# Optimization experiments

Hardware: AMD Instinct MI355X
Metric: run time of the kernel (lower is better)

## Reference

```python
import jax, jax.numpy as jnp
import numpy as np
from jax import lax

D_MODEL = 1024
N_HEADS = 16
D_HEAD = D_MODEL // N_HEADS  # 64
NB_FEAT = 266
CHUNK = 128
KERNEL_EPS = 1e-4
CAUSAL_EPS = 1e-6


def _gaussian_orthogonal_matrix(nb_rows, nb_cols, seed=0):
    # Performer gaussian_orthogonal_random_matrix, scaling=0:
    # stacked orthogonal blocks scaled by chi-distributed row norms.
    rng = np.random.default_rng(seed)
    blocks = []
    n_full = nb_rows // nb_cols + (1 if nb_rows % nb_cols else 0)
    for _ in range(n_full):
        g = rng.standard_normal((nb_cols, nb_cols))
        q_mat, _ = np.linalg.qr(g)
        blocks.append(q_mat.T)
    mat = np.concatenate(blocks, axis=0)[:nb_rows]
    multiplier = np.linalg.norm(rng.standard_normal((nb_rows, nb_cols)), axis=1)
    return jnp.asarray((multiplier[:, None] * mat).astype(np.float32))


def setup_inputs() -> dict:
    key = jax.random.key(0)
    ks = jax.random.split(key, 9)
    s = 1.0 / np.sqrt(D_MODEL)
    x = jax.random.normal(ks[0], (2, 4096, D_MODEL), dtype=jnp.float32)
    def lin(k):
        kw, kb = jax.random.split(k)
        W = jax.random.uniform(kw, (D_MODEL, D_MODEL), jnp.float32, -s, s)
        b = jax.random.uniform(kb, (D_MODEL,), jnp.float32, -s, s)
        return W, b
    Wq, bq = lin(ks[1]); Wk, bk = lin(ks[2]); Wv, bv = lin(ks[3]); Wo, bo = lin(ks[4])
    proj = _gaussian_orthogonal_matrix(NB_FEAT, D_HEAD)
    return {"x": x, "Wq": Wq, "bq": bq, "Wk": Wk, "bk": bk, "Wv": Wv, "bv": bv,
            "Wo": Wo, "bo": bo, "proj": proj}


def _softmax_kernel(data, proj, is_query):
    # Performer random-feature softmax kernel.
    data_normalizer = data.shape[-1] ** -0.25
    ratio = proj.shape[0] ** -0.5
    dn = data * data_normalizer  # [b,h,n,d]
    data_dash = jnp.einsum('bhnd,md->bhnm', dn, proj)
    diag = 0.5 * jnp.sum(dn * dn, axis=-1, keepdims=True)  # [b,h,n,1]
    if is_query:
        stab = jnp.max(data_dash, axis=-1, keepdims=True)
    else:
        stab = jnp.max(data_dash)
    return ratio * (jnp.exp(data_dash - diag - stab) + KERNEL_EPS)


def _causal_linear_attention(qp, kp, v, chunk_size):
    # Chunked O(n) causal linear attention (Performer noncuda variant).
    b, h, n, m = qp.shape
    d = v.shape[-1]
    nc = n // chunk_size
    qc = jnp.moveaxis(qp.reshape(b, h, nc, chunk_size, m), 2, 0)  # [nc,b,h,c,m]
    kc = jnp.moveaxis(kp.reshape(b, h, nc, chunk_size, m), 2, 0)
    vc = jnp.moveaxis(v.reshape(b, h, nc, chunk_size, d), 2, 0)   # [nc,b,h,c,d]

    def step(carry, inp):
        last_k, last_ctx = carry  # [b,h,m], [b,h,m,d]
        q, k, vv = inp
        k_cum = last_k[:, :, None, :] + jnp.cumsum(k, axis=-2)          # [b,h,c,m]
        D_inv = 1.0 / jnp.einsum('bhcm,bhcm->bhc', q, k_cum + CAUSAL_EPS)
        ctx = jnp.einsum('bhcm,bhcd->bhcmd', k, vv)                     # [b,h,c,m,d]
        ctx_cum = last_ctx[:, :, None, :, :] + jnp.cumsum(ctx, axis=2)
        out = jnp.einsum('bhcmd,bhcm,bhc->bhcd', ctx_cum, q, D_inv)
        return (k_cum[:, :, -1, :], ctx_cum[:, :, -1, :, :]), out

    carry0 = (jnp.zeros((b, h, m), qp.dtype), jnp.zeros((b, h, m, d), qp.dtype))
    _, outs = lax.scan(step, carry0, (qc, kc, vc))  # [nc,b,h,c,d]
    return jnp.moveaxis(outs, 0, 2).reshape(b, h, n, d)


def reference(x, Wq, bq, Wk, bk, Wv, bv, Wo, bo, proj):
    bsz, n, _ = x.shape
    def split_heads(t):
        return t.reshape(bsz, n, N_HEADS, D_HEAD).transpose(0, 2, 1, 3)  # [b,h,n,d]
    q = split_heads(x @ Wq.T + bq)
    k = split_heads(x @ Wk.T + bk)
    v = split_heads(x @ Wv.T + bv)
    q_prime = _softmax_kernel(q, proj, is_query=True)
    k_prime = _softmax_kernel(k, proj, is_query=False)
    attn = _causal_linear_attention(q_prime, k_prime, v, CHUNK)  # [b,h,n,d]
    attn = attn.transpose(0, 2, 1, 3).reshape(bsz, n, D_MODEL)
    return attn @ Wo.T + bo
```

## Files before the change

kernel.cpp:

```cpp
#include <hip/hip_runtime.h>

#define B_    2
#define NSEQ  4096
#define DM    1024
#define H_    16
#define DH    64
#define MF    266
#define MP    288
#define NROWS (B_*NSEQ)
#define NHROWS (B_*H_*NSEQ)
#define RATIO 0.06131393394849658f
#define DNORM 0.3535533905932738f
#define KEPS  1e-4f
#define CEPS  1e-6f

#define CH    128
#define NC    32
#define SROW  (65*MP)
#define SELEM (64*MP)

#define AS1 __attribute__((address_space(1)))
#define AS3 __attribute__((address_space(3)))

typedef unsigned short u16;
typedef unsigned int   u32;

typedef __bf16 bf16x8 __attribute__((ext_vector_type(8)));
typedef float  f32x4  __attribute__((ext_vector_type(4)));

__device__ __forceinline__ float b2f(u16 u){ u32 x = ((u32)u) << 16; return __builtin_bit_cast(float, x); }
__device__ __forceinline__ u16 f2b(float f){
    u32 x = __builtin_bit_cast(u32, f);
    u32 r = x + 0x7fffu + ((x >> 16) & 1u);
    return (u16)(r >> 16);
}
__device__ __forceinline__ u32 enc_max(float f){ u32 b = __builtin_bit_cast(u32, f); return (b & 0x80000000u) ? ~b : (b | 0x80000000u); }
__device__ __forceinline__ float dec_max(u32 u){ u32 b = (u & 0x80000000u) ? (u & 0x7fffffffu) : ~u; return __builtin_bit_cast(float, b); }

struct DetectArgs { const u32* p[10]; int nw[10]; };

__global__ void detect_all(DetectArgs a, u32* __restrict__ flags)
{
    __shared__ int cnt[256];
    int k = blockIdx.x;
    const u32* src = a.p[k];
    int nwords = a.nw[k];
    int t = threadIdx.x; int c = 0;
    for (int i = t; i < nwords; i += 256) {
        u32 w = src[i];
        int ea = (int)((w >> 7)  & 0xFF);
        int eb = (int)((w >> 23) & 0xFF);
        c += (ea >= 112 && ea <= 143) ? 1 : 0;
        c += (eb >= 112 && eb <= 143) ? 1 : 0;
    }
    cnt[t] = c; __syncthreads();
    for (int s = 128; s; s >>= 1) { if (t < s) cnt[t] += cnt[t + s]; __syncthreads(); }
    if (t == 0) flags[k] = (cnt[0] >= (nwords * 3) / 2) ? 1u : 0u;
}

__device__ __forceinline__ void conv8(const void* src, u16* dst, int i, u32 flag)
{
    if (flag) {
        *(uint4*)(dst + i) = *(const uint4*)((const u16*)src + i);
    } else {
        const float* s = (const float*)src + i;
        u16 tmp[8];
        #pragma unroll
        for (int j = 0; j < 8; ++j) tmp[j] = f2b(s[j]);
        *(uint4*)(dst + i) = *(uint4*)tmp;
    }
}

struct ConvAllArgs {
    const void* xs;    u16* xd;
    const void* wsrc[4]; u16* wdst[4];
    const void* bsrc[4]; u16* bdst[4];
    const void* pj;    u16* pjd;
    u32* gpart; u32* gmax;
    const u32* flags;
};

__global__ __launch_bounds__(256)
void conv_all(ConvAllArgs a)
{
    int blk = blockIdx.x, t = threadIdx.x;
    if (blk < 4096) {
        int i = blk * 2048 + t * 8;
        conv8(a.xs, a.xd, i, a.flags[0]);
    } else if (blk < 6144) {
        int r = blk - 4096; int w = r >> 9; int i = (r & 511) * 2048 + t * 8;
        conv8(a.wsrc[w], a.wdst[w], i, a.flags[1 + 2*w]);
    } else if (blk < 6148) {
        int w = blk - 6144; int i = t * 8;
        if (i < DM) conv8(a.bsrc[w], a.bdst[w], i, a.flags[2 + 2*w]);
    } else if (blk < 6157) {
        int i = (blk - 6148) * 2048 + t * 8;
        if (i < MF * DH) conv8(a.pj, a.pjd, i, a.flags[9]);
        else             *(uint4*)(a.pjd + i) = (uint4){0,0,0,0};
    } else {
        a.gpart[t] = 0u;
        if (t == 0) *a.gmax = 0u;
    }
}

#define GEMM_BODY(A_, Bm_, ACC_)                                              \
    const int K = DM;                                                          \
    __shared__ u16 As[128 * 32];                                               \
    __shared__ u16 Bs[128 * 32];                                               \
    int t = threadIdx.x;                                                       \
    int wave = t >> 6, lane = t & 63;                                          \
    int wm = wave >> 1, wn = wave & 1;                                         \
    int quad = lane >> 4, l16 = lane & 15;                                     \
    int bm = blockIdx.x * 128, bn = blockIdx.y * 128;                          \
    int rA0 = (wave*2 + 0)*16 + (lane >> 2);                                   \
    int rA1 = (wave*2 + 1)*16 + (lane >> 2);                                   \
    int cs0 = ((lane & 3) ^ (rA0 & 3)) * 8;                                    \
    int cs1 = ((lane & 3) ^ (rA1 & 3)) * 8;                                    \
    const u16* a0 = A_  + (size_t)(bm + rA0) * K + cs0;                        \
    const u16* a1 = A_  + (size_t)(bm + rA1) * K + cs1;                        \
    const u16* b0 = Bm_ + (size_t)(bn + rA0) * K + cs0;                        \
    const u16* b1 = Bm_ + (size_t)(bn + rA1) * K + cs1;                        \
    u16* la0 = As + (wave*2 + 0)*512;                                          \
    u16* la1 = As + (wave*2 + 1)*512;                                          \
    u16* lb0 = Bs + (wave*2 + 0)*512;                                          \
    u16* lb1 = Bs + (wave*2 + 1)*512;                                          \
    f32x4 ACC_[4][4];                                                          \
    _Pragma("unroll")                                                          \
    for (int i = 0; i < 4; ++i)                                                \
        _Pragma("unroll")                                                      \
        for (int j = 0; j < 4; ++j) ACC_[i][j] = (f32x4){0.f,0.f,0.f,0.f};     \
    for (int k0 = 0; k0 < K; k0 += 32) {                                       \
        __builtin_amdgcn_global_load_lds((const AS1 void*)(a0 + k0), (AS3 void*)la0, 16, 0, 0); \
        __builtin_amdgcn_global_load_lds((const AS1 void*)(a1 + k0), (AS3 void*)la1, 16, 0, 0); \
        __builtin_amdgcn_global_load_lds((const AS1 void*)(b0 + k0), (AS3 void*)lb0, 16, 0, 0); \
        __builtin_amdgcn_global_load_lds((const AS1 void*)(b1 + k0), (AS3 void*)lb1, 16, 0, 0); \
        __syncthreads();                                                       \
        bf16x8 af[4], bfr[4];                                                  \
        int qsw = (quad ^ (l16 & 3)) << 4;                                     \
        _Pragma("unroll")                                                      \
        for (int i = 0; i < 4; ++i) {                                          \
            af[i]  = *(const bf16x8*)((const char*)As + (wm*64 + i*16 + l16)*64 + qsw); \
            bfr[i] = *(const bf16x8*)((const char*)Bs + (wn*64 + i*16 + l16)*64 + qsw); \
        }                                                                      \
        _Pragma("unroll")                                                      \
        for (int i = 0; i < 4; ++i)                                            \
            _Pragma("unroll")                                                  \
            for (int j = 0; j < 4; ++j)                                        \
                ACC_[i][j] = __builtin_amdgcn_mfma_f32_16x16x32_bf16(af[i], bfr[j], ACC_[i][j], 0, 0, 0); \
        __syncthreads();                                                       \
    }

__global__ __launch_bounds__(256)
void gemm_qkv(const u16* __restrict__ A,
              const u16* __restrict__ Wqb, const u16* __restrict__ Wkb,
              const u16* __restrict__ Wvb,
              const u16* __restrict__ bqb, const u16* __restrict__ bkb,
              const u16* __restrict__ bvb,
              u16* __restrict__ Vb, float* __restrict__ Qf, float* __restrict__ Kf)
{
    int z = blockIdx.z;
    const u16* Bm   = (z == 0) ? Wvb : (z == 1) ? Wqb : Wkb;
    const u16* bias = (z == 0) ? bvb : (z == 1) ? bqb : bkb;
    GEMM_BODY(A, Bm, acc)
    float* Of = (z == 1) ? Qf : Kf;
    #pragma unroll
    for (int i = 0; i < 4; ++i) {
        #pragma unroll
        for (int j = 0; j < 4; ++j) {
            int col = bn + wn*64 + j*16 + l16;
            float bv = b2f(bias[col]);
            #pragma unroll
            for (int r = 0; r < 4; ++r) {
                int row = bm + wm*64 + i*16 + quad*4 + r;
                float v = acc[i][j][r] + bv;
                if (z == 0) Vb[(size_t)row * DM + col] = f2b(v);
                else        Of[(size_t)row * DM + col] = v;
            }
        }
    }
}

template<int OUT_BF16>
__global__ __launch_bounds__(256)
void gemm_nt(const u16* __restrict__ A, const u16* __restrict__ Bm,
             const u16* __restrict__ bias, void* __restrict__ C)
{
    GEMM_BODY(A, Bm, acc)
    #pragma unroll
    for (int i = 0; i < 4; ++i) {
        #pragma unroll
        for (int j = 0; j < 4; ++j) {
            int col = bn + wn*64 + j*16 + l16;
            float bv = b2f(bias[col]);
            #pragma unroll
            for (int r = 0; r < 4; ++r) {
                int row = bm + wm*64 + i*16 + quad*4 + r;
                float v = acc[i][j][r] + bv;
                if (OUT_BF16) ((u16*)C)[(size_t)row * DM + col] = f2b(v);
                else          ((float*)C)[(size_t)row * DM + col] = v;
            }
        }
    }
}

template<int MODE>
__global__ __launch_bounds__(256)
void feat_mfma(const float* __restrict__ X, const u16* __restrict__ projP,
               u16* __restrict__ OutP, u32* __restrict__ gpart,
               const u32* __restrict__ gmax)
{
    int blk = blockIdx.x;
    int bh = blk >> 6, nt = blk & 63;
    int b = bh >> 4, h = bh & 15;
    int n0 = nt * 64;
    int t = threadIdx.x;
    int lane = t & 63, w = t >> 6;
    int quad = lane >> 4, l16 = lane & 15;

    __shared__ uint4 smemU[2368];
    __shared__ float red4[4];
    u16* smem16 = (u16*)smemU;

    const float* xrow = X + ((size_t)(b * NSEQ + n0 + w*16 + l16)) * DM + h * DH;
    float va[2][8];
    #pragma unroll
    for (int ks = 0; ks < 2; ++ks) {
        float4 u0 = *(const float4*)(xrow + ks*32 + quad*8);
        float4 u1 = *(const float4*)(xrow + ks*32 + quad*8 + 4);
        va[ks][0]=u0.x; va[ks][1]=u0.y; va[ks][2]=u0.z; va[ks][3]=u0.w;
        va[ks][4]=u1.x; va[ks][5]=u1.y; va[ks][6]=u1.z; va[ks][7]=u1.w;
    }

    for (int i = t; i < 2304; i += 256) {
        int m = i >> 3, c = i & 7;
        uint4 v = *(const uint4*)(projP + m*64 + c*8);
        int dstb = m*128 + ((c*16) ^ ((m & 7) << 4));
        *(uint4*)((char*)smemU + dstb) = v;
    }

    bf16x8 ahi[2], alo[2];
    float sq = 0.f;
    #pragma unroll
    for (int ks = 0; ks < 2; ++ks) {
        #pragma unroll
        for (int i = 0; i < 8; ++i) {
            float v = va[ks][i] * DNORM;
            sq += v * v;
            u16 hb = f2b(v);
            float hv = b2f(hb);
            ahi[ks][i] = __builtin_bit_cast(__bf16, hb);
            alo[ks][i] = __builtin_bit_cast(__bf16, f2b(v - hv));
        }
    }
    sq += __shfl_xor(sq, 16, 64);
    sq += __shfl_xor(sq, 32, 64);
    float diag_my = 0.5f * sq;

    __syncthreads();

    f32x4 acc[18];
    #pragma unroll
    for (int j = 0; j < 18; ++j) acc[j] = (f32x4){0.f,0.f,0.f,0.f};
    #pragma unroll
    for (int j = 0; j < 18; ++j) {
        int m = j*16 + l16;
        #pragma unroll
        for (int ks = 0; ks < 2; ++ks) {
            int off = m*128 + (((quad*16) + ks*64) ^ ((m & 7) << 4));
            bf16x8 bf = *(const bf16x8*)((const char*)smemU + off);
            acc[j] = __builtin_amdgcn_mfma_f32_16x16x32_bf16(ahi[ks], bf, acc[j], 0, 0, 0);
            acc[j] = __builtin_amdgcn_mfma_f32_16x16x32_bf16(alo[ks], bf, acc[j], 0, 0, 0);
        }
    }

    float rmax[4];
    #pragma unroll
    for (int r = 0; r < 4; ++r) rmax[r] = -3.4e38f;
    #pragma unroll
    for (int j = 0; j < 16; ++j)
        #pragma unroll
        for (int r = 0; r < 4; ++r) rmax[r] = fmaxf(rmax[r], acc[j][r]);
    if (l16 < MF - 256) {
        #pragma unroll
        for (int r = 0; r < 4; ++r) rmax[r] = fmaxf(rmax[r], acc[16][r]);
    }
    #pragma unroll
    for (int s = 1; s < 16; s <<= 1)
        #pragma unroll
        for (int r = 0; r < 4; ++r)
            rmax[r] = fmaxf(rmax[r], __shfl_xor(rmax[r], s, 64));

    if (MODE == 1) {
        float wm2 = fmaxf(fmaxf(rmax[0], rmax[1]), fmaxf(rmax[2], rmax[3]));
        wm2 = fmaxf(wm2, __shfl_xor(wm2, 16, 64));
        wm2 = fmaxf(wm2, __shfl_xor(wm2, 32, 64));
        if (lane == 0) red4[w] = wm2;
        __syncthreads();
        if (t == 0) {
            float bm2 = fmaxf(fmaxf(red4[0], red4[1]), fmaxf(red4[2], red4[3]));
            atomicMax(&gpart[blk & 255], enc_max(bm2));
        }
        return;
    }

    float gstab = (MODE == 2) ? dec_max(*gmax) : 0.f;
    float dg[4];
    #pragma unroll
    for (int r = 0; r < 4; ++r) dg[r] = __shfl(diag_my, quad*4 + r, 64);

    __syncthreads();

    #pragma unroll
    for (int j = 0; j < 18; ++j) {
        int m = j*16 + l16;
        #pragma unroll
        for (int r = 0; r < 4; ++r) {
            float stab = (MODE == 0) ? rmax[r] : gstab;
            float val = RATIO * (__expf(acc[j][r] - dg[r] - stab) + KEPS);
            u16 ov = (m < MF) ? f2b(val) : (u16)0;
            smem16[(w*16 + quad*4 + r) * 296 + m] = ov;
        }
    }
    __syncthreads();

    u16* obase = OutP + ((size_t)bh * NSEQ + n0) * MP;
    for (int i = t; i < 2304; i += 256) {
        int row = i / 36, c = i - row * 36;
        *(uint4*)(obase + row*MP + c*8) = *(const uint4*)(smem16 + row*296 + c*8);
    }
}

__global__ void gmax_reduce(const u32* __restrict__ gpart, u32* __restrict__ gmax)
{
    __shared__ u32 r[256];
    int t = threadIdx.x;
    r[t] = gpart[t]; __syncthreads();
    for (int s = 128; s; s >>= 1) { if (t < s) r[t] = max(r[t], r[t + s]); __syncthreads(); }
    if (t == 0) *gmax = r[0];
}

__global__ __launch_bounds__(256)
void chunk_ST(const u16* __restrict__ Kp, const u16* __restrict__ Vb,
              u16* __restrict__ Sb, float* __restrict__ zf)
{
    int bhc = blockIdx.x;
    int bh = bhc >> 5, c = bhc & (NC - 1);
    int b = bh >> 4, h = bh & 15;
    int t = threadIdx.x, w = t >> 6, lane = t & 63;
    int quad = lane >> 4, l16 = lane & 15;
    int n0 = c * CH;

    __shared__ __align__(16) u16 KTs[288*72];
    __shared__ __align__(16) u16 VTs[80*136];

    {
        int d0 = (t >> 5) * 8, nb = (t & 31) * 4;
        const u16* vb2 = Vb + ((size_t)(b*NSEQ + n0 + nb)) * DM + h*DH + d0;
        uint4 r0 = *(const uint4*)(vb2);
        uint4 r1 = *(const uint4*)(vb2 + DM);
        uint4 r2 = *(const uint4*)(vb2 + 2*DM);
        uint4 r3 = *(const uint4*)(vb2 + 3*DM);
        const u32* a0 = (const u32*)&r0; const u32* a1 = (const u32*)&r1;
        const u32* a2 = (const u32*)&r2; const u32* a3 = (const u32*)&r3;
        #pragma unroll
        for (int e = 0; e < 8; ++e) {
            u32 w0 = a0[e>>1], w1 = a1[e>>1], w2 = a2[e>>1], w3 = a3[e>>1];
            u32 lo2, hi2;
            if (e & 1) { lo2 = (w0 >> 16) | (w1 & 0xFFFF0000u); hi2 = (w2 >> 16) | (w3 & 0xFFFF0000u); }
            else       { lo2 = (w0 & 0xFFFFu) | (w1 << 16);     hi2 = (w2 & 0xFFFFu) | (w3 << 16); }
            uint2 uu; uu.x = lo2; uu.y = hi2;
            *(uint2*)&VTs[(d0 + e)*136 + nb] = uu;
        }
        if (t < 128) VTs[64*136 + t] = 0x3F80u;
        if (t < 255) {
            int rr = 65 + t/17, cc2 = t - (t/17)*17;
            uint4 z4 = (uint4){0,0,0,0};
            *(uint4*)&VTs[rr*136 + cc2*8] = z4;
        }
    }

    f32x4 am[18], az[5];
    #pragma unroll
    for (int mt = 0; mt < 18; ++mt) am[mt] = (f32x4){0.f,0.f,0.f,0.f};
    #pragma unroll
    for (int j = 0; j < 5; ++j) az[j] = (f32x4){0.f,0.f,0.f,0.f};

    const u16* kbase = Kp + ((size_t)bh * NSEQ + n0) * MP;
    for (int h2 = 0; h2 < 2; ++h2) {
        __syncthreads();
        for (int i = t; i < 576; i += 256) {
            int nb4 = (i & 15) * 4, m0 = (i >> 4) * 8;
            const u16* kb = kbase + (size_t)(h2*64 + nb4) * MP + m0;
            uint4 r0 = *(const uint4*)(kb);
            uint4 r1 = *(const uint4*)(kb + MP);
            uint4 r2 = *(const uint4*)(kb + 2*MP);
            uint4 r3 = *(const uint4*)(kb + 3*MP);
            const u32* a0 = (const u32*)&r0; const u32* a1 = (const u32*)&r1;
            const u32* a2 = (const u32*)&r2; const u32* a3 = (const u32*)&r3;
            #pragma unroll
            for (int e = 0; e < 8; ++e) {
                u32 w0 = a0[e>>1], w1 = a1[e>>1], w2 = a2[e>>1], w3 = a3[e>>1];
                u32 lo2, hi2;
                if (e & 1) { lo2 = (w0 >> 16) | (w1 & 0xFFFF0000u); hi2 = (w2 >> 16) | (w3 & 0xFFFF0000u); }
                else       { lo2 = (w0 & 0xFFFFu) | (w1 << 16);     hi2 = (w2 & 0xFFFFu) | (w3 << 16); }
                uint2 uu; uu.x = lo2; uu.y = hi2;
                *(uint2*)&KTs[(m0 + e)*72 + nb4] = uu;
            }
        }
        __syncthreads();
        #pragma unroll
        for (int ks = 0; ks < 2; ++ks) {
            int nof = h2*64 + ks*32 + quad*8;
            bf16x8 aw = *(const bf16x8*)&VTs[(w*16 + l16)*136 + nof];
            bf16x8 a4 = *(const bf16x8*)&VTs[(64 + l16)*136 + nof];
            #pragma unroll
            for (int mt = 0; mt < 18; ++mt) {
                bf16x8 bk = *(const bf16x8*)&KTs[(mt*16 + l16)*72 + ks*32 + quad*8];
                am[mt] = __builtin_amdgcn_mfma_f32_16x16x32_bf16(aw, bk, am[mt], 0, 0, 0);
            }
            #pragma unroll
            for (int j = 0; j < 5; ++j) {
                int mtz = w + 4*j;
                if (mtz < 18) {
                    bf16x8 bk = *(const bf16x8*)&KTs[(mtz*16 + l16)*72 + ks*32 + quad*8];
                    az[j] = __builtin_amdgcn_mfma_f32_16x16x32_bf16(a4, bk, az[j], 0, 0, 0);
                }
            }
        }
    }

    u16* sb = Sb + (size_t)bhc * SELEM;
    #pragma unroll
    for (int mt = 0; mt < 18; ++mt)
        #pragma unroll
        for (int r = 0; r < 4; ++r)
            sb[(size_t)(w*16 + quad*4 + r) * MP + mt*16 + l16] = f2b(am[mt][r]);
    if (quad == 0) {
        #pragma unroll
        for (int j = 0; j < 5; ++j) {
            int mtz = w + 4*j;
            if (mtz < 18) zf[(size_t)bhc * MP + mtz*16 + l16] = az[j][0];
        }
    }
}

__global__ __launch_bounds__(256)
void chunk_prefix(u16* __restrict__ Sb, float* __restrict__ zf)
{
    int gid = blockIdx.x * 256 + threadIdx.x;
    int bh = gid / SROW;
    int rem = gid - bh * SROW;
    float run = 0.f;
    if (rem < SELEM) {
        size_t base = (size_t)(bh * NC) * SELEM + rem;
        #pragma unroll 4
        for (int c2 = 0; c2 < NC; ++c2) {
            size_t o = base + (size_t)c2 * SELEM;
            float v = b2f(Sb[o]);
            Sb[o] = f2b(run);
            run += v;
        }
    } else {
        int m = rem - SELEM;
        size_t base = (size_t)(bh * NC) * MP + m;
        #pragma unroll 4
        for (int c2 = 0; c2 < NC; ++c2) {
            size_t o = base + (size_t)c2 * MP;
            float v = zf[o];
            zf[o] = run + CEPS;
            run += v;
        }
    }
}

__global__ __launch_bounds__(256)
void scan_mfma(const u16* __restrict__ Qp, const u16* __restrict__ Kp,
               const u16* __restrict__ Vb, const u16* __restrict__ Sb,
               const float* __restrict__ zf, u16* __restrict__ attn)
{
    int bhc = blockIdx.x;
    int bh = bhc >> 5, c = bhc & (NC - 1);
    int b = bh >> 4, h = bh & 15;
    int t = threadIdx.x, w = t >> 6, lane = t & 63;
    int quad = lane >> 4, l16 = lane & 15;
    int n0 = c * CH;
    int it0 = w, it1 = 7 - w;

    __shared__ __align__(16) u16 R1s[9472];
    __shared__ __align__(16) u16 R2s[18944];

    for (int i = t; i < 2176; i += 256) ((uint4*)R2s)[i] = (uint4){0,0,0,0};

    bf16x8 q0[9], q1[9];
    {
        const u16* qa = Qp + ((size_t)bh * NSEQ + n0 + it0*16 + l16) * MP + quad*8;
        const u16* qb = Qp + ((size_t)bh * NSEQ + n0 + it1*16 + l16) * MP + quad*8;
        #pragma unroll
        for (int s = 0; s < 9; ++s) {
            q0[s] = *(const bf16x8*)(qa + s*32);
            q1[s] = *(const bf16x8*)(qb + s*32);
        }
    }

    float denw0 = 0.f, denw1 = 0.f;
    const u16* kbase = Kp + ((size_t)bh * NSEQ + n0) * MP;

    for (int qt = 0; qt < 4; ++qt) {
        __syncthreads();
        for (int i = t; i < 1152; i += 256) {
            int rr = i / 36, cc = i - rr * 36;
            *(uint4*)&R1s[rr*296 + cc*8] =
                *(const uint4*)(kbase + (size_t)(qt*32 + rr) * MP + cc*8);
        }
        __syncthreads();
        #pragma unroll
        for (int jj = 0; jj < 2; ++jj) {
            int jt = qt*2 + jj;
            #pragma unroll
            for (int itx = 0; itx < 2; ++itx) {
                int it = itx ? it1 : it0;
                if (jt <= it) {
                    f32x4 acc = (f32x4){0.f,0.f,0.f,0.f};
                    #pragma unroll
                    for (int s = 0; s < 9; ++s) {
                        bf16x8 kf = *(const bf16x8*)&R1s[(jj*16 + l16)*296 + s*32 + quad*8];
                        acc = __builtin_amdgcn_mfma_f32_16x16x32_bf16(
                            kf, itx ? q1[s] : q0[s], acc, 0, 0, 0);
                    }
                    int ig = it*16 + l16;
                    float rs = 0.f;
                    #pragma unroll
                    for (int r = 0; r < 4; ++r) {
                        int jg = jt*16 + quad*4 + r;
                        float pv = (jg <= ig) ? acc[r] : 0.f;
                        rs += pv;
                        R2s[ig*136 + jg] = f2b(pv);
                    }
                    if (itx) denw1 += rs; else denw0 += rs;
                }
            }
        }
    }

    __syncthreads();
    {
        int d0 = (t >> 5) * 8, nb = (t & 31) * 4;
        const u16* vb2 = Vb + ((size_t)(b*NSEQ + n0 + nb)) * DM + h*DH + d0;
        uint4 r0 = *(const uint4*)(vb2);
        uint4 r1 = *(const uint4*)(vb2 + DM);
        uint4 r2 = *(const uint4*)(vb2 + 2*DM);
        uint4 r3 = *(const uint4*)(vb2 + 3*DM);
        const u32* a0 = (const u32*)&r0; const u32* a1 = (const u32*)&r1;
        const u32* a2 = (const u32*)&r2; const u32* a3 = (const u32*)&r3;
        #pragma unroll
        for (int e = 0; e < 8; ++e) {
            u32 w0 = a0[e>>1], w1 = a1[e>>1], w2 = a2[e>>1], w3 = a3[e>>1];
            u32 lo2, hi2;
            if (e & 1) { lo2 = (w0 >> 16) | (w1 & 0xFFFF0000u); hi2 = (w2 >> 16) | (w3 & 0xFFFF0000u); }
            else       { lo2 = (w0 & 0xFFFFu) | (w1 << 16);     hi2 = (w2 & 0xFFFFu) | (w3 << 16); }
            uint2 uu; uu.x = lo2; uu.y = hi2;
            *(uint2*)&R1s[(d0 + e)*136 + nb] = uu;
        }
    }
    __syncthreads();

    f32x4 pacc[2][4];
    #pragma unroll
    for (int i = 0; i < 2; ++i)
        #pragma unroll
        for (int j = 0; j < 4; ++j) pacc[i][j] = (f32x4){0.f,0.f,0.f,0.f};
    int ns0 = (it0 + 2) >> 1, ns1 = (it1 + 2) >> 1;
    #pragma unroll
    for (int ks = 0; ks < 4; ++ks) {
        bool u0 = ks < ns0, u1 = ks < ns1;
        bf16x8 p0 = {}, p1 = {};
        if (u0) p0 = *(const bf16x8*)&R2s[(it0*16 + l16)*136 + ks*32 + quad*8];
        if (u1) p1 = *(const bf16x8*)&R2s[(it1*16 + l16)*136 + ks*32 + quad*8];
        #pragma unroll
        for (int ct = 0; ct < 4; ++ct) {
            bf16x8 vf = *(const bf16x8*)&R1s[(ct*16 + l16)*136 + ks*32 + quad*8];
            if (u0) pacc[0][ct] = __builtin_amdgcn_mfma_f32_16x16x32_bf16(p0, vf, pacc[0][ct], 0, 0, 0);
            if (u1) pacc[1][ct] = __builtin_amdgcn_mfma_f32_16x16x32_bf16(p1, vf, pacc[1][ct], 0, 0, 0);
        }
    }

    f32x4 cacc[2][4];
    #pragma unroll
    for (int i = 0; i < 2; ++i)
        #pragma unroll
        for (int j = 0; j < 4; ++j) cacc[i][j] = (f32x4){0.f,0.f,0.f,0.f};
    const u16* sbw = Sb + (size_t)bhc * SELEM;
    __syncthreads();
    for (int i = t; i < 2304; i += 256) {
        int rr = i / 36, cc = i - rr * 36;
        *(uint4*)&R2s[rr*296 + cc*8] = *(const uint4*)(sbw + (size_t)rr * MP + cc*8);
    }
    __syncthreads();
    #pragma unroll
    for (int s = 0; s < 9; ++s)
        #pragma unroll
        for (int ct = 0; ct < 4; ++ct) {
            bf16x8 sf = *(const bf16x8*)&R2s[(ct*16 + l16)*296 + s*32 + quad*8];
            cacc[0][ct] = __builtin_amdgcn_mfma_f32_16x16x32_bf16(q0[s], sf, cacc[0][ct], 0, 0, 0);
            cacc[1][ct] = __builtin_amdgcn_mfma_f32_16x16x32_bf16(q1[s], sf, cacc[1][ct], 0, 0, 0);
        }

    float dc0 = 0.f, dc1 = 0.f;
    {
        const float* zc = zf + (size_t)bhc * MP + quad*8;
        #pragma unroll
        for (int s = 0; s < 9; ++s) {
            f32x4 za = *(const f32x4*)(zc + s*32);
            f32x4 zb = *(const f32x4*)(zc + s*32 + 4);
            #pragma unroll
            for (int e = 0; e < 4; ++e) {
                dc0 += (float)q0[s][e] * za[e];
                dc0 += (float)q0[s][e+4] * zb[e];
                dc1 += (float)q1[s][e] * za[e];
                dc1 += (float)q1[s][e+4] * zb[e];
            }
        }
    }
    dc0 += __shfl_xor(dc0, 16, 64); dc0 += __shfl_xor(dc0, 32, 64);
    dc1 += __shfl_xor(dc1, 16, 64); dc1 += __shfl_xor(dc1, 32, 64);
    denw0 += __shfl_xor(denw0, 16, 64); denw0 += __shfl_xor(denw0, 32, 64);
    denw1 += __shfl_xor(denw1, 16, 64); denw1 += __shfl_xor(denw1, 32, 64);
    float den0 = denw0 + dc0, den1 = denw1 + dc1;

    u16* ab = attn + ((size_t)(b*NSEQ + n0)) * DM + h*DH;
    #pragma unroll
    for (int itx = 0; itx < 2; ++itx) {
        int it = itx ? it1 : it0;
        float dv = itx ? den1 : den0;
        #pragma unroll
        for (int r = 0; r < 4; ++r) {
            float deno = __shfl(dv, (lane & 48) + quad*4 + r, 64);
            int row = it*16 + quad*4 + r;
            #pragma unroll
            for (int ct = 0; ct < 4; ++ct) {
                float ov = (pacc[itx][ct][r] + cacc[itx][ct][r]) / deno;
                ab[(size_t)row * DM + ct*16 + l16] = f2b(ov);
            }
        }
    }
}

extern "C" void kernel_launch(void* const* d_in, const int* in_sizes, int n_in,
                              void* d_out, int out_size, void* d_ws, size_t ws_size,
                              hipStream_t stream)
{
    (void)n_in; (void)out_size; (void)ws_size;
    const void* x  = d_in[0];
    const void* Wq = d_in[1]; const void* bq = d_in[2];
    const void* Wk = d_in[3]; const void* bk = d_in[4];
    const void* Wv = d_in[5]; const void* bv = d_in[6];
    const void* Wo = d_in[7]; const void* bo = d_in[8];
    const void* proj = d_in[9];

    char* ws = (char*)d_ws;
    size_t off = 0;
    auto alloc = [&](size_t bytes) -> char* {
        char* p = ws + off; off += (bytes + 255) & ~(size_t)255; return p;
    };
    size_t qkfBytes = (size_t)NROWS * DM * 4;
    size_t sbBytes  = (size_t)(B_ * H_ * NC) * SELEM * 2;
    size_t zfBytes  = (size_t)(B_ * H_ * NC) * MP * 4;
    size_t ovBytes  = 2 * qkfBytes;
    if (sbBytes + zfBytes > ovBytes) ovBytes = sbBytes + zfBytes;
    char*  ov0  = alloc(ovBytes);
    float* QKf0 = (float*)ov0;
    float* QKf1 = (float*)(ov0 + qkfBytes);
    u16*   Sb   = (u16*)ov0;
    float* zfp  = (float*)(ov0 + sbBytes);
    u16*   Vb   = (u16*)alloc((size_t)NROWS * DM * 2);
    u16*   Qp   = (u16*)alloc((size_t)NHROWS * MP * 2);
    u16*   Kp   = (u16*)alloc((size_t)NHROWS * MP * 2);
    u16*   projC= (u16*)alloc((size_t)MP * DH * 2);
    u16*   Wqb  = (u16*)alloc((size_t)DM * DM * 2);
    u16*   Wkb  = (u16*)alloc((size_t)DM * DM * 2);
    u16*   Wvb  = (u16*)alloc((size_t)DM * DM * 2);
    u16*   Wob  = (u16*)alloc((size_t)DM * DM * 2);
    u16*   bqb  = (u16*)alloc(DM * 2);
    u16*   bkb  = (u16*)alloc(DM * 2);
    u16*   bvb  = (u16*)alloc(DM * 2);
    u16*   bob  = (u16*)alloc(DM * 2);
    u32*   flags= (u32*)alloc(16 * 4);
    u32*   gmax = (u32*)alloc(256);
    u32*   gpart= (u32*)alloc(256 * 4);
    char*  xatt = alloc((size_t)NROWS * DM * 2);
    u16*   xb   = (u16*)xatt;
    u16*   attn = (u16*)xatt;

    DetectArgs da;
    for (int i = 0; i < 10; ++i) {
        int n = in_sizes[i];
        int nwords = n / 2; if (nwords > 4096) nwords = 4096;
        da.p[i] = (const u32*)d_in[i];
        da.nw[i] = nwords;
    }
    detect_all<<<10, 256, 0, stream>>>(da, flags);

    ConvAllArgs ca;
    ca.xs = x;  ca.xd = xb;
    ca.wsrc[0] = Wq; ca.wsrc[1] = Wk; ca.wsrc[2] = Wv; ca.wsrc[3] = Wo;
    ca.wdst[0] = Wqb; ca.wdst[1] = Wkb; ca.wdst[2] = Wvb; ca.wdst[3] = Wob;
    ca.bsrc[0] = bq; ca.bsrc[1] = bk; ca.bsrc[2] = bv; ca.bsrc[3] = bo;
    ca.bdst[0] = bqb; ca.bdst[1] = bkb; ca.bdst[2] = bvb; ca.bdst[3] = bob;
    ca.pj = proj; ca.pjd = projC;
    ca.gpart = gpart; ca.gmax = gmax; ca.flags = flags;
    conv_all<<<6158, 256, 0, stream>>>(ca);

    dim3 gq(NROWS / 128, DM / 128, 3);
    gemm_qkv<<<gq, 256, 0, stream>>>(xb, Wqb, Wkb, Wvb, bqb, bkb, bvb, Vb, QKf0, QKf1);

    feat_mfma<0><<<NHROWS / 64, 256, 0, stream>>>(QKf0, projC, Qp, gpart, gmax);
    feat_mfma<1><<<NHROWS / 64, 256, 0, stream>>>(QKf1, projC, Kp, gpart, gmax);
    gmax_reduce<<<1, 256, 0, stream>>>(gpart, gmax);
    feat_mfma<2><<<NHROWS / 64, 256, 0, stream>>>(QKf1, projC, Kp, gpart, gmax);

    chunk_ST<<<B_ * H_ * NC, 256, 0, stream>>>(Kp, Vb, Sb, zfp);
    chunk_prefix<<<(B_ * H_ * SROW) / 256, 256, 0, stream>>>(Sb, zfp);
    scan_mfma<<<B_ * H_ * NC, 256, 0, stream>>>(Qp, Kp, Vb, Sb, zfp, attn);

    dim3 gg(NROWS / 128, DM / 128);
    gemm_nt<0><<<gg, 256, 0, stream>>>(attn, Wob, bob, d_out);
}
```

Measured before the change: 388.5 us.

## Deepen GEMM K-tile, swizzle QKV grid per XCD, shrink scan/chunk LDS

New measurement: 389.3 us. About the same (+0.2%).

```diff
diff --git a/kernel.cpp b/kernel.cpp
--- a/kernel.cpp
+++ b/kernel.cpp
@@ -103,50 +103,48 @@
     }
 }
 
-#define GEMM_BODY(A_, Bm_, ACC_)                                              \
+#define GEMM_BODY(A_, Bm_, bm_, bn_, ACC_)                                    \
     const int K = DM;                                                          \
-    __shared__ u16 As[128 * 32];                                               \
-    __shared__ u16 Bs[128 * 32];                                               \
+    __shared__ u16 As[128 * 64];                                               \
+    __shared__ u16 Bs[128 * 64];                                               \
     int t = threadIdx.x;                                                       \
     int wave = t >> 6, lane = t & 63;                                          \
     int wm = wave >> 1, wn = wave & 1;                                         \
     int quad = lane >> 4, l16 = lane & 15;                                     \
-    int bm = blockIdx.x * 128, bn = blockIdx.y * 128;                          \
-    int rA0 = (wave*2 + 0)*16 + (lane >> 2);                                   \
-    int rA1 = (wave*2 + 1)*16 + (lane >> 2);                                   \
-    int cs0 = ((lane & 3) ^ (rA0 & 3)) * 8;                                    \
-    int cs1 = ((lane & 3) ^ (rA1 & 3)) * 8;                                    \
-    const u16* a0 = A_  + (size_t)(bm + rA0) * K + cs0;                        \
-    const u16* a1 = A_  + (size_t)(bm + rA1) * K + cs1;                        \
-    const u16* b0 = Bm_ + (size_t)(bn + rA0) * K + cs0;                        \
-    const u16* b1 = Bm_ + (size_t)(bn + rA1) * K + cs1;                        \
-    u16* la0 = As + (wave*2 + 0)*512;                                          \
-    u16* la1 = As + (wave*2 + 1)*512;                                          \
-    u16* lb0 = Bs + (wave*2 + 0)*512;                                          \
-    u16* lb1 = Bs + (wave*2 + 1)*512;                                          \
+    int rowc = lane >> 3;                                                      \
+    int csrc = ((lane & 7) ^ rowc) * 8;                                        \
+    int cA = wave * 4;                                                         \
+    const u16* ap0 = A_  + (size_t)(bm_ + cA*8 + rowc) * K + csrc;             \
+    const u16* bp0 = Bm_ + (size_t)(bn_ + cA*8 + rowc) * K + csrc;             \
+    u16* lA = As + cA * 512;                                                   \
+    u16* lB = Bs + cA * 512;                                                   \
     f32x4 ACC_[4][4];                                                          \
     _Pragma("unroll")                                                          \
     for (int i = 0; i < 4; ++i)                                                \
         _Pragma("unroll")                                                      \
         for (int j = 0; j < 4; ++j) ACC_[i][j] = (f32x4){0.f,0.f,0.f,0.f};     \
-    for (int k0 = 0; k0 < K; k0 += 32) {                                       \
-        __builtin_amdgcn_global_load_lds((const AS1 void*)(a0 + k0), (AS3 void*)la0, 16, 0, 0); \
-        __builtin_amdgcn_global_load_lds((const AS1 void*)(a1 + k0), (AS3 void*)la1, 16, 0, 0); \
-        __builtin_amdgcn_global_load_lds((const AS1 void*)(b0 + k0), (AS3 void*)lb0, 16, 0, 0); \
-        __builtin_amdgcn_global_load_lds((const AS1 void*)(b1 + k0), (AS3 void*)lb1, 16, 0, 0); \
+    for (int k0 = 0; k0 < K; k0 += 64) {                                       \
+        _Pragma("unroll")                                                      \
+        for (int j = 0; j < 4; ++j) {                                          \
+            __builtin_amdgcn_global_load_lds((const AS1 void*)(ap0 + (size_t)j*8*K + k0), (AS3 void*)(lA + j*512), 16, 0, 0); \
+            __builtin_amdgcn_global_load_lds((const AS1 void*)(bp0 + (size_t)j*8*K + k0), (AS3 void*)(lB + j*512), 16, 0, 0); \
+        }                                                                      \
         __syncthreads();                                                       \
-        bf16x8 af[4], bfr[4];                                                  \
-        int qsw = (quad ^ (l16 & 3)) << 4;                                     \
         _Pragma("unroll")                                                      \
-        for (int i = 0; i < 4; ++i) {                                          \
-            af[i]  = *(const bf16x8*)((const char*)As + (wm*64 + i*16 + l16)*64 + qsw); \
-            bfr[i] = *(const bf16x8*)((const char*)Bs + (wn*64 + i*16 + l16)*64 + qsw); \
+        for (int ks = 0; ks < 2; ++ks) {                                       \
+            bf16x8 af[4], bfr[4];                                              \
+            int sw = ((((ks << 2) | quad) ^ (l16 & 7)) << 4);                  \
+            _Pragma("unroll")                                                  \
+            for (int i = 0; i < 4; ++i) {                                      \
+                af[i]  = *(const bf16x8*)((const char*)As + (wm*64 + i*16 + l16)*128 + sw); \
+                bfr[i] = *(const bf16x8*)((const char*)Bs + (wn*64 + i*16 + l16)*128 + sw); \
+            }                                                                  \
+            _Pragma("unroll")                                                  \
+            for (int i = 0; i < 4; ++i)                                        \
+                _Pragma("unroll")                                              \
+                for (int j = 0; j < 4; ++j)                                    \
+                    ACC_[i][j] = __builtin_amdgcn_mfma_f32_16x16x32_bf16(af[i], bfr[j], ACC_[i][j], 0, 0, 0); \
         }                                                                      \
-        _Pragma("unroll")                                                      \
-        for (int i = 0; i < 4; ++i)                                            \
-            _Pragma("unroll")                                                  \
-            for (int j = 0; j < 4; ++j)                                        \
-                ACC_[i][j] = __builtin_amdgcn_mfma_f32_16x16x32_bf16(af[i], bfr[j], ACC_[i][j], 0, 0, 0); \
         __syncthreads();                                                       \
     }
 
@@ -158,10 +156,19 @@
               const u16* __restrict__ bvb,
               u16* __restrict__ Vb, float* __restrict__ Qf, float* __restrict__ Kf)
 {
-    int z = blockIdx.z;
+    int bid = blockIdx.x;
+    int xcd = bid & 7, pos = bid >> 3;
+    int lb  = xcd * 192 + pos;
+    int z   = lb % 3;
+    int q   = lb / 3;
+    int idx = q & 15, sg = q >> 4;
+    int sgm = sg & 15, sgn = sg >> 4;
+    int bm = (sgm*4 + (idx & 3)) * 128;
+    int bn = (sgn*4 + (idx >> 2)) * 128;
+
     const u16* Bm   = (z == 0) ? Wvb : (z == 1) ? Wqb : Wkb;
     const u16* bias = (z == 0) ? bvb : (z == 1) ? bqb : bkb;
-    GEMM_BODY(A, Bm, acc)
+    GEMM_BODY(A, Bm, bm, bn, acc)
     float* Of = (z == 1) ? Qf : Kf;
     #pragma unroll
     for (int i = 0; i < 4; ++i) {
@@ -185,7 +192,8 @@
 void gemm_nt(const u16* __restrict__ A, const u16* __restrict__ Bm,
              const u16* __restrict__ bias, void* __restrict__ C)
 {
-    GEMM_BODY(A, Bm, acc)
+    int bm = blockIdx.x * 128, bn = blockIdx.y * 128;
+    GEMM_BODY(A, Bm, bm, bn, acc)
     #pragma unroll
     for (int i = 0; i < 4; ++i) {
         #pragma unroll
@@ -350,7 +358,7 @@
     int quad = lane >> 4, l16 = lane & 15;
     int n0 = c * CH;
 
-    __shared__ __align__(16) u16 KTs[288*72];
+    __shared__ __align__(16) u16 KTs[288*40];
     __shared__ __align__(16) u16 VTs[80*136];
 
     {
@@ -386,11 +394,11 @@
     for (int j = 0; j < 5; ++j) az[j] = (f32x4){0.f,0.f,0.f,0.f};
 
     const u16* kbase = Kp + ((size_t)bh * NSEQ + n0) * MP;
-    for (int h2 = 0; h2 < 2; ++h2) {
+    for (int qh = 0; qh < 4; ++qh) {
         __syncthreads();
-        for (int i = t; i < 576; i += 256) {
-            int nb4 = (i & 15) * 4, m0 = (i >> 4) * 8;
-            const u16* kb = kbase + (size_t)(h2*64 + nb4) * MP + m0;
+        for (int i = t; i < 288; i += 256) {
+            int nb4 = (i & 7) * 4, m0 = (i >> 3) * 8;
+            const u16* kb = kbase + (size_t)(qh*32 + nb4) * MP + m0;
             uint4 r0 = *(const uint4*)(kb);
             uint4 r1 = *(const uint4*)(kb + MP);
             uint4 r2 = *(const uint4*)(kb + 2*MP);
@@ -404,27 +412,24 @@
                 if (e & 1) { lo2 = (w0 >> 16) | (w1 & 0xFFFF0000u); hi2 = (w2 >> 16) | (w3 & 0xFFFF0000u); }
                 else       { lo2 = (w0 & 0xFFFFu) | (w1 << 16);     hi2 = (w2 & 0xFFFFu) | (w3 << 16); }
                 uint2 uu; uu.x = lo2; uu.y = hi2;
-                *(uint2*)&KTs[(m0 + e)*72 + nb4] = uu;
+                *(uint2*)&KTs[(m0 + e)*40 + nb4] = uu;
             }
         }
         __syncthreads();
-        #pragma unroll
-        for (int ks = 0; ks < 2; ++ks) {
-            int nof = h2*64 + ks*32 + quad*8;
-            bf16x8 aw = *(const bf16x8*)&VTs[(w*16 + l16)*136 + nof];
-            bf16x8 a4 = *(const bf16x8*)&VTs[(64 + l16)*136 + nof];
-            #pragma unroll
-            for (int mt = 0; mt < 18; ++mt) {
-                bf16x8 bk = *(const bf16x8*)&KTs[(mt*16 + l16)*72 + ks*32 + quad*8];
-                am[mt] = __builtin_amdgcn_mfma_f32_16x16x32_bf16(aw, bk, am[mt], 0, 0, 0);
-            }
-            #pragma unroll
-            for (int j = 0; j < 5; ++j) {
-                int mtz = w + 4*j;
-                if (mtz < 18) {
-                    bf16x8 bk = *(const bf16x8*)&KTs[(mtz*16 + l16)*72 + ks*32 + quad*8];
-                    az[j] = __builtin_amdgcn_mfma_f32_16x16x32_bf16(a4, bk, az[j], 0, 0, 0);
-                }
+        int nof = qh*32 + quad*8;
+        bf16x8 aw = *(const bf16x8*)&VTs[(w*16 + l16)*136 + nof];
+        bf16x8 a4 = *(const bf16x8*)&VTs[(64 + l16)*136 + nof];
+        #pragma unroll
+        for (int mt = 0; mt < 18; ++mt) {
+            bf16x8 bk = *(const bf16x8*)&KTs[(mt*16 + l16)*40 + quad*8];
+            am[mt] = __builtin_amdgcn_mfma_f32_16x16x32_bf16(aw, bk, am[mt], 0, 0, 0);
+        }
+        #pragma unroll
+        for (int j = 0; j < 5; ++j) {
+            int mtz = w + 4*j;
+            if (mtz < 18) {
+                bf16x8 bk = *(const bf16x8*)&KTs[(mtz*16 + l16)*40 + quad*8];
+                az[j] = __builtin_amdgcn_mfma_f32_16x16x32_bf16(a4, bk, az[j], 0, 0, 0);
             }
         }
     }
@@ -487,7 +492,7 @@
     int it0 = w, it1 = 7 - w;
 
     __shared__ __align__(16) u16 R1s[9472];
-    __shared__ __align__(16) u16 R2s[18944];
+    __shared__ __align__(16) u16 R2s[17408];
 
     for (int i = t; i < 2176; i += 256) ((uint4*)R2s)[i] = (uint4){0,0,0,0};
 
@@ -590,20 +595,24 @@
         #pragma unroll
         for (int j = 0; j < 4; ++j) cacc[i][j] = (f32x4){0.f,0.f,0.f,0.f};
     const u16* sbw = Sb + (size_t)bhc * SELEM;
-    __syncthreads();
-    for (int i = t; i < 2304; i += 256) {
-        int rr = i / 36, cc = i - rr * 36;
-        *(uint4*)&R2s[rr*296 + cc*8] = *(const uint4*)(sbw + (size_t)rr * MP + cc*8);
-    }
-    __syncthreads();
-    #pragma unroll
-    for (int s = 0; s < 9; ++s)
-        #pragma unroll
-        for (int ct = 0; ct < 4; ++ct) {
-            bf16x8 sf = *(const bf16x8*)&R2s[(ct*16 + l16)*296 + s*32 + quad*8];
-            cacc[0][ct] = __builtin_amdgcn_mfma_f32_16x16x32_bf16(q0[s], sf, cacc[0][ct], 0, 0, 0);
-            cacc[1][ct] = __builtin_amdgcn_mfma_f32_16x16x32_bf16(q1[s], sf, cacc[1][ct], 0, 0, 0);
-        }
+    #pragma unroll
+    for (int p = 0; p < 2; ++p) {
+        __syncthreads();
+        for (int i = t; i < 1152; i += 256) {
+            int rr = i / 36, cc = i - rr * 36;
+            *(uint4*)&R1s[rr*296 + cc*8] =
+                *(const uint4*)(sbw + (size_t)(p*32 + rr) * MP + cc*8);
+        }
+        __syncthreads();
+        #pragma unroll
+        for (int s = 0; s < 9; ++s)
+            #pragma unroll
+            for (int cl = 0; cl < 2; ++cl) {
+                bf16x8 sf = *(const bf16x8*)&R1s[(cl*16 + l16)*296 + s*32 + quad*8];
+                cacc[0][p*2 + cl] = __builtin_amdgcn_mfma_f32_16x16x32_bf16(q0[s], sf, cacc[0][p*2 + cl], 0, 0, 0);
+                cacc[1][p*2 + cl] = __builtin_amdgcn_mfma_f32_16x16x32_bf16(q1[s], sf, cacc[1][p*2 + cl], 0, 0, 0);
+            }
+    }
 
     float dc0 = 0.f, dc1 = 0.f;
     {
@@ -710,8 +719,7 @@
     ca.gpart = gpart; ca.gmax = gmax; ca.flags = flags;
     conv_all<<<6158, 256, 0, stream>>>(ca);
 
-    dim3 gq(NROWS / 128, DM / 128, 3);
-    gemm_qkv<<<gq, 256, 0, stream>>>(xb, Wqb, Wkb, Wvb, bqb, bkb, bvb, Vb, QKf0, QKf1);
+    gemm_qkv<<<1536, 256, 0, stream>>>(xb, Wqb, Wkb, Wvb, bqb, bkb, bvb, Vb, QKf0, QKf1);
 
     feat_mfma<0><<<NHROWS / 64, 256, 0, stream>>>(QKf0, projC, Qp, gpart, gmax);
     feat_mfma<1><<<NHROWS / 64, 256, 0, stream>>>(QKf1, projC, Kp, gpart, gmax);
```
